# Kernel tuning notes

Hardware: AMD Instinct MI355X
Metric: run time of the kernel (lower is better)

Reference implementation:

```python
import jax, jax.numpy as jnp
import numpy as np

B, S, E, H = 2, 2048, 1024, 16
D = E // H  # head size

def setup_inputs() -> dict:
    key = jax.random.key(0)
    ks = jax.random.split(key, 11)
    s = 0.02
    return {
        "q": jax.random.normal(ks[0], (B, S, E), jnp.float32),
        "k": jax.random.normal(ks[1], (B, S, E), jnp.float32),
        "v": jax.random.normal(ks[2], (B, S, E), jnp.float32),
        "Wq": jax.random.normal(ks[3], (E, E), jnp.float32) * s,
        "bq": jax.random.normal(ks[4], (E,), jnp.float32) * s,
        "Wk": jax.random.normal(ks[5], (E, E), jnp.float32) * s,
        "bk": jax.random.normal(ks[6], (E,), jnp.float32) * s,
        "Wv": jax.random.normal(ks[7], (E, E), jnp.float32) * s,
        "bv": jax.random.normal(ks[8], (E,), jnp.float32) * s,
        "Wo": jax.random.normal(ks[9], (E, E), jnp.float32) * s,
        "bo": jax.random.normal(ks[10], (E,), jnp.float32) * s,
    }

def reference(q, k, v, Wq, bq, Wk, bk, Wv, bv, Wo, bo):
    b, sq, _ = q.shape
    sk = k.shape[1]
    # linear projections, split into heads: [B,S,H,D]
    qh = (q @ Wq.T + bq).reshape(b, sq, H, D)
    kh = (k @ Wk.T + bk).reshape(b, sk, H, D)
    vh = (v @ Wv.T + bv).reshape(b, sk, H, D)
    # NOTE: original module does NOT scale by 1/sqrt(D)
    scores = jnp.einsum('bqhe,bkhe->bhqk', qh, kh)
    probs = jax.nn.softmax(scores, axis=-1)  # dropout = identity (eval)
    attn = jnp.einsum('bhqk,bkhe->bqhe', probs, vh).reshape(b, sq, E)
    return attn @ Wo.T + bo
```

## Files before the change

### kernel.cpp

```cpp
#include <hip/hip_runtime.h>
#include <stdint.h>

#define BH 2
#define SEQ 2048
#define EMB 1024
#define NH 16
#define HD 64
#define MROWS (BH * SEQ)
#define BHN (BH * NH)
#define LOG2E 1.44269504f

typedef __attribute__((ext_vector_type(8))) short bf16x8;
typedef __attribute__((ext_vector_type(4))) float f32x4;
typedef __attribute__((ext_vector_type(16))) float f32x16;

static __device__ __forceinline__ unsigned short f2bf(float x) {
  union { float f; unsigned int u; } a; a.f = x;
  unsigned int r = a.u + 0x7fffu + ((a.u >> 16) & 1u);
  return (unsigned short)(r >> 16);
}

static __device__ __forceinline__ unsigned int cvtpk(float lo, float hi) {
  unsigned int r;
  asm("v_cvt_pk_bf16_f32 %0, %1, %2" : "=v"(r) : "v"(lo), "v"(hi));
  return r;
}

static __device__ __forceinline__ float vexp2(float x) {
  float r;
  asm("v_exp_f32 %0, %1" : "=v"(r) : "v"(x));
  return r;
}

static __device__ __forceinline__ void plswap(unsigned int& a, unsigned int& b) {
  asm volatile("v_permlane32_swap_b32 %0, %1" : "+v"(a), "+v"(b));
}

struct Conv7 { const float* s[7]; unsigned short* d[7]; };

__global__ __launch_bounds__(256) void conv_all(Conv7 a) {
  const int b = blockIdx.x;
  int r, off;
  if (b < 12288) { r = b >> 12; off = b & 4095; }
  else { int t = b - 12288; r = 3 + (t >> 10); off = t & 1023; }
  const int i = (off * 256 + threadIdx.x) * 4;
  float4 v = *(const float4*)(a.s[r] + i);
  ushort4 o;
  o.x = f2bf(v.x); o.y = f2bf(v.y); o.z = f2bf(v.z); o.w = f2bf(v.w);
  *(ushort4*)(a.d[r] + i) = o;
}

struct B3 { const float* p[3]; };
struct Out3 { void* p[3]; };

template <int MODE>
__global__ __launch_bounds__(256) void gemm128(const unsigned short* __restrict__ Abase,
                                               const unsigned short* __restrict__ Bbase,
                                               B3 biases, Out3 outs) {
  __shared__ unsigned short lsm[128 * 128];
  unsigned short* lA = lsm;
  unsigned short* lB = lsm + 128 * 64;
  const int z = blockIdx.z;
  const unsigned short* A  = Abase + (size_t)z * MROWS * EMB;
  const unsigned short* Bt = Bbase + (size_t)z * EMB * EMB;
  const float* bias = biases.p[z];
  const int tid = threadIdx.x;
  const int lane = tid & 63;
  const int w = tid >> 6;
  const int row0 = blockIdx.x * 128;
  const int col0 = blockIdx.y * 128;
  const int wr = (w >> 1) * 64;
  const int wc = (w & 1) * 64;
  const int r16 = lane & 15;
  const int g = lane >> 4;

  const int s_rowoff = (lane >> 3);
  const int s_col = ((lane & 7) ^ s_rowoff) * 8;

  f32x4 acc[4][4] = {};

  for (int kt = 0; kt < EMB / 64; ++kt) {
    const int k0 = kt * 64;
    __syncthreads();
#pragma unroll
    for (int j = 0; j < 4; ++j) {
      const int chunk = w * 4 + j;
      const int row = chunk * 8 + s_rowoff;
      __builtin_amdgcn_global_load_lds(
          (const __attribute__((address_space(1))) void*)(A + (size_t)(row0 + row) * EMB + k0 + s_col),
          (__attribute__((address_space(3))) void*)(lA + chunk * 512), 16, 0, 0);
      __builtin_amdgcn_global_load_lds(
          (const __attribute__((address_space(1))) void*)(Bt + (size_t)(col0 + row) * EMB + k0 + s_col),
          (__attribute__((address_space(3))) void*)(lB + chunk * 512), 16, 0, 0);
    }
    __syncthreads();
#pragma unroll
    for (int kk = 0; kk < 2; ++kk) {
      bf16x8 a[4], b[4];
#pragma unroll
      for (int m = 0; m < 4; ++m) {
        const int row = wr + m * 16 + r16;
        a[m] = *(const bf16x8*)(lA + row * 64 + (((kk << 2) + g) ^ (r16 & 7)) * 8);
      }
#pragma unroll
      for (int n = 0; n < 4; ++n) {
        const int row = wc + n * 16 + r16;
        b[n] = *(const bf16x8*)(lB + row * 64 + (((kk << 2) + g) ^ (r16 & 7)) * 8);
      }
#pragma unroll
      for (int m = 0; m < 4; ++m)
#pragma unroll
        for (int n = 0; n < 4; ++n)
          acc[m][n] = __builtin_amdgcn_mfma_f32_16x16x32_bf16(a[m], b[n], acc[m][n], 0, 0, 0);
    }
  }

  if (MODE == 1) {
#pragma unroll
    for (int m = 0; m < 4; ++m)
#pragma unroll
      for (int n = 0; n < 4; ++n) {
        const int colg = col0 + wc + n * 16 + r16;
        const float bv = bias[colg];
#pragma unroll
        for (int j = 0; j < 4; ++j) {
          const int rowg = row0 + wr + m * 16 + g * 4 + j;
          ((float*)outs.p[0])[(size_t)rowg * EMB + colg] = acc[m][n][j] + bv;
        }
      }
  } else {
    const int b_ = row0 >> 11;
    const int s0 = row0 & 2047;
    const int h0 = col0 >> 6;
    const float scl = (z == 0) ? LOG2E : 1.0f;
    if (z != 2) {
#pragma unroll
      for (int half = 0; half < 2; ++half) {
        __syncthreads();
        if ((w >> 1) == half) {
#pragma unroll
          for (int m = 0; m < 4; ++m)
#pragma unroll
            for (int n = 0; n < 4; ++n) {
              const int cl = wc + n * 16 + r16;
              const float bv = bias[col0 + cl];
#pragma unroll
              for (int j = 0; j < 4; ++j)
                lsm[(m * 16 + g * 4 + j) * 136 + cl] = f2bf((acc[m][n][j] + bv) * scl);
            }
        }
        __syncthreads();
        const int rr_ = tid >> 2, q4 = tid & 3;
        const int h_ = h0 + (q4 >> 1);
        unsigned short* dst = (unsigned short*)outs.p[z] +
            ((size_t)(b_ * NH + h_) * SEQ + s0 + half * 64 + rr_) * 64 + (q4 & 1) * 32;
        uint4 x0 = *(uint4*)&lsm[rr_ * 136 + q4 * 32];
        uint4 x1 = *(uint4*)&lsm[rr_ * 136 + q4 * 32 + 8];
        uint4 x2 = *(uint4*)&lsm[rr_ * 136 + q4 * 32 + 16];
        uint4 x3 = *(uint4*)&lsm[rr_ * 136 + q4 * 32 + 24];
        *(uint4*)dst = x0;
        *(uint4*)(dst + 8) = x1;
        *(uint4*)(dst + 16) = x2;
        *(uint4*)(dst + 24) = x3;
      }
    } else {
#pragma unroll
      for (int half = 0; half < 2; ++half) {
        __syncthreads();
        if ((w >> 1) == half) {
#pragma unroll
          for (int m = 0; m < 4; ++m)
#pragma unroll
            for (int n = 0; n < 4; ++n) {
              const int cl = wc + n * 16 + r16;
              const float bv = bias[col0 + cl];
#pragma unroll
              for (int j = 0; j < 4; ++j)
                lsm[cl * 72 + m * 16 + g * 4 + j] = f2bf(acc[m][n][j] + bv);
            }
        }
        __syncthreads();
        const int c_ = tid >> 1, sh = tid & 1;
        const int h_ = h0 + (c_ >> 6);
        const int d_ = c_ & 63;
        unsigned short* dst = (unsigned short*)outs.p[2] +
            ((size_t)(b_ * NH + h_) * HD + d_) * SEQ + s0 + half * 64 + sh * 32;
        uint4 y0 = *(uint4*)&lsm[c_ * 72 + sh * 32];
        uint4 y1 = *(uint4*)&lsm[c_ * 72 + sh * 32 + 8];
        uint4 y2 = *(uint4*)&lsm[c_ * 72 + sh * 32 + 16];
        uint4 y3 = *(uint4*)&lsm[c_ * 72 + sh * 32 + 24];
        *(uint4*)dst = y0;
        *(uint4*)(dst + 8) = y1;
        *(uint4*)(dst + 16) = y2;
        *(uint4*)(dst + 24) = y3;
      }
    }
  }
}

__global__ __launch_bounds__(256) void attn_fwd(const unsigned short* __restrict__ Qh,
                                                const unsigned short* __restrict__ Kh,
                                                const unsigned short* __restrict__ Vt,
                                                unsigned short* __restrict__ ctx) {
  __shared__ unsigned short kbuf[2][64 * 64];
  __shared__ unsigned short vbuf[2][64 * 64];
  const int tid = threadIdx.x;
  const int lane = tid & 63;
  const int w = tid >> 6;
  const int l31 = lane & 31;
  const int hi = lane >> 5;
  const int wg = blockIdx.x;
  const int xcd = wg & 7;
  const int slot = wg >> 3;
  const int bh = xcd + 8 * (slot >> 4);
  const int qb = slot & 15;
  const size_t base = (size_t)bh * SEQ * HD;
  const unsigned short* Q = Qh + base;
  const unsigned short* K = Kh + base;
  const unsigned short* V = Vt + base;
  const int q0 = qb * 128 + w * 32;

  bf16x8 bq[4];
#pragma unroll
  for (int ks = 0; ks < 4; ++ks)
    bq[ks] = *(const bf16x8*)(Q + (size_t)(q0 + l31) * HD + ks * 16 + hi * 8);

  f32x16 oacc0 = {};
  f32x16 oacc1 = {};
  float lsum = 0.f;

  const int sr = tid >> 2;
  const int sx = (tid & 3) * 2;
  const int sd0 = ((sx) ^ (sr & 7)) * 8;
  const int sd1 = ((sx + 1) ^ (sr & 7)) * 8;

  const int NT = SEQ / 64;
  uint4 kr0, kr1, vr0, vr1;
  kr0 = *(const uint4*)(K + (size_t)sr * HD + sx * 8);
  kr1 = *(const uint4*)(K + (size_t)sr * HD + sx * 8 + 8);
  vr0 = *(const uint4*)(V + (size_t)sr * SEQ + sx * 8);
  vr1 = *(const uint4*)(V + (size_t)sr * SEQ + sx * 8 + 8);
  *(uint4*)(kbuf[0] + sr * 64 + sd0) = kr0;
  *(uint4*)(kbuf[0] + sr * 64 + sd1) = kr1;
  *(uint4*)(vbuf[0] + sr * 64 + sd0) = vr0;
  *(uint4*)(vbuf[0] + sr * 64 + sd1) = vr1;
  kr0 = *(const uint4*)(K + (size_t)(64 + sr) * HD + sx * 8);
  kr1 = *(const uint4*)(K + (size_t)(64 + sr) * HD + sx * 8 + 8);
  vr0 = *(const uint4*)(V + (size_t)sr * SEQ + 64 + sx * 8);
  vr1 = *(const uint4*)(V + (size_t)sr * SEQ + 64 + sx * 8 + 8);
  __syncthreads();

  for (int t = 0; t < NT; ++t) {
    const unsigned short* lK = kbuf[t & 1];
    const unsigned short* lV = vbuf[t & 1];
#pragma unroll
    for (int sub = 0; sub < 2; ++sub) {
      f32x16 st = {};
      __builtin_amdgcn_s_setprio(1);
#pragma unroll
      for (int ks = 0; ks < 4; ++ks) {
        bf16x8 ak = *(const bf16x8*)(lK + (sub * 32 + l31) * 64 +
                                     (((ks << 1) + hi) ^ (l31 & 7)) * 8);
        st = __builtin_amdgcn_mfma_f32_32x32x16_bf16(ak, bq[ks], st, 0, 0, 0);
      }
      __builtin_amdgcn_s_setprio(0);
      float p[16];
#pragma unroll
      for (int r = 0; r < 16; ++r) { p[r] = vexp2(st[r]); lsum += p[r]; }
#pragma unroll
      for (int h2 = 0; h2 < 2; ++h2) {
        const int b8 = h2 * 8;
        unsigned int a0 = cvtpk(p[b8 + 0], p[b8 + 1]);
        unsigned int b0 = cvtpk(p[b8 + 4], p[b8 + 5]);
        unsigned int a1 = cvtpk(p[b8 + 2], p[b8 + 3]);
        unsigned int b1 = cvtpk(p[b8 + 6], p[b8 + 7]);
        plswap(a0, b0);
        plswap(a1, b1);
        union { unsigned int u[4]; bf16x8 v; } pa;
        pa.u[0] = a0; pa.u[1] = a1; pa.u[2] = b0; pa.u[3] = b1;
        const int kst = sub * 2 + h2;
        const int vsl = (((kst << 1) + hi) ^ (l31 & 7)) * 8;
        bf16x8 v0 = *(const bf16x8*)(lV + l31 * 64 + vsl);
        bf16x8 v1 = *(const bf16x8*)(lV + (32 + l31) * 64 + vsl);
        __builtin_amdgcn_s_setprio(1);
        oacc0 = __builtin_amdgcn_mfma_f32_32x32x16_bf16(pa.v, v0, oacc0, 0, 0, 0);
        oacc1 = __builtin_amdgcn_mfma_f32_32x32x16_bf16(pa.v, v1, oacc1, 0, 0, 0);
        __builtin_amdgcn_s_setprio(0);
      }
    }
    if (t + 1 < NT) {
      unsigned short* nK = kbuf[(t + 1) & 1];
      unsigned short* nV = vbuf[(t + 1) & 1];
      *(uint4*)(nK + sr * 64 + sd0) = kr0;
      *(uint4*)(nK + sr * 64 + sd1) = kr1;
      *(uint4*)(nV + sr * 64 + sd0) = vr0;
      *(uint4*)(nV + sr * 64 + sd1) = vr1;
      if (t + 2 < NT) {
        const int kv2 = (t + 2) * 64;
        kr0 = *(const uint4*)(K + (size_t)(kv2 + sr) * HD + sx * 8);
        kr1 = *(const uint4*)(K + (size_t)(kv2 + sr) * HD + sx * 8 + 8);
        vr0 = *(const uint4*)(V + (size_t)sr * SEQ + kv2 + sx * 8);
        vr1 = *(const uint4*)(V + (size_t)sr * SEQ + kv2 + sx * 8 + 8);
      }
    }
    __syncthreads();
  }

  lsum += __shfl_xor(lsum, 32, 64);
  const float linv = 1.0f / lsum;
  const int b_ = bh >> 4, h_ = bh & 15;
#pragma unroll
  for (int reg = 0; reg < 16; ++reg) {
    const int crow = (reg & 3) + 8 * (reg >> 2) + 4 * hi;
    const float rv = __shfl(linv, crow, 64);
    const size_t rowaddr = ((size_t)(b_ * SEQ + q0 + crow) << 10) + h_ * 64 + l31;
    ctx[rowaddr]      = f2bf(oacc0[reg] * rv);
    ctx[rowaddr + 32] = f2bf(oacc1[reg] * rv);
  }
}

extern "C" void kernel_launch(void* const* d_in, const int* in_sizes, int n_in,
                              void* d_out, int out_size, void* d_ws, size_t ws_size,
                              hipStream_t stream) {
  const float* q  = (const float*)d_in[0];
  const float* k  = (const float*)d_in[1];
  const float* v  = (const float*)d_in[2];
  const float* Wq = (const float*)d_in[3];
  const float* bq = (const float*)d_in[4];
  const float* Wk = (const float*)d_in[5];
  const float* bk = (const float*)d_in[6];
  const float* Wv = (const float*)d_in[7];
  const float* bv = (const float*)d_in[8];
  const float* Wo = (const float*)d_in[9];
  const float* bo = (const float*)d_in[10];

  char* ws = (char*)d_ws;
  const size_t SZ_ACT = (size_t)MROWS * EMB * 2;
  const size_t SZ_W   = (size_t)EMB * EMB * 2;
  unsigned short* qb  = (unsigned short*)(ws);
  unsigned short* kb  = (unsigned short*)(ws + SZ_ACT);
  unsigned short* vb  = (unsigned short*)(ws + 2 * SZ_ACT);
  unsigned short* Wqb = (unsigned short*)(ws + 3 * SZ_ACT);
  unsigned short* Wob = (unsigned short*)(ws + 3 * SZ_ACT + 3 * SZ_W);
  unsigned short* Qh  = (unsigned short*)(ws + 3 * SZ_ACT + 4 * SZ_W);
  unsigned short* Kh  = (unsigned short*)(ws + 4 * SZ_ACT + 4 * SZ_W);
  unsigned short* Vt  = (unsigned short*)(ws + 5 * SZ_ACT + 4 * SZ_W);
  unsigned short* ctx = (unsigned short*)(ws + 6 * SZ_ACT + 4 * SZ_W);

  Conv7 ca;
  ca.s[0] = q;  ca.s[1] = k;  ca.s[2] = v;
  ca.s[3] = Wq; ca.s[4] = Wk; ca.s[5] = Wv; ca.s[6] = Wo;
  ca.d[0] = qb; ca.d[1] = kb; ca.d[2] = vb;
  ca.d[3] = Wqb; ca.d[4] = Wqb + EMB * EMB; ca.d[5] = Wqb + 2 * EMB * EMB; ca.d[6] = Wob;
  conv_all<<<16384, 256, 0, stream>>>(ca);

  B3 bqkv; bqkv.p[0] = bq; bqkv.p[1] = bk; bqkv.p[2] = bv;
  Out3 oqkv; oqkv.p[0] = (void*)Qh; oqkv.p[1] = (void*)Kh; oqkv.p[2] = (void*)Vt;
  gemm128<0><<<dim3(MROWS / 128, EMB / 128, 3), 256, 0, stream>>>(qb, Wqb, bqkv, oqkv);

  attn_fwd<<<512, 256, 0, stream>>>(Qh, Kh, Vt, ctx);

  B3 bout; bout.p[0] = bo; bout.p[1] = bo; bout.p[2] = bo;
  Out3 oout; oout.p[0] = d_out; oout.p[1] = d_out; oout.p[2] = d_out;
  gemm128<1><<<dim3(MROWS / 128, EMB / 128, 1), 256, 0, stream>>>(ctx, Wob, bout, oout);
}
```

Before: 231.0 us.

## Use 128x64 GEMM tiles and 128-key attention tiles with paired score MFMAs

The projection GEMMs now use a 128x64 output tile instead of 128x128, doubling the grid size for better CU occupancy and simplifying the head-scatter epilogue to a single LDS pass. The attention kernel stages 128 keys per double-buffered tile instead of 64, halving the number of barriers and issuing two independent score MFMA chains per step for more ILP. Row sums are accumulated with a tree reduction. The cost is more LDS in attention and lower A-reuse per GEMM tile.

```diff
diff --git a/kernel.cpp b/kernel.cpp
--- a/kernel.cpp
+++ b/kernel.cpp
@@ -57,7 +57,7 @@
 __global__ __launch_bounds__(256) void gemm128(const unsigned short* __restrict__ Abase,
                                                const unsigned short* __restrict__ Bbase,
                                                B3 biases, Out3 outs) {
-  __shared__ unsigned short lsm[128 * 128];
+  __shared__ unsigned short lsm[128 * 64 + 64 * 64];
   unsigned short* lA = lsm;
   unsigned short* lB = lsm + 128 * 64;
   const int z = blockIdx.z;
@@ -68,16 +68,16 @@
   const int lane = tid & 63;
   const int w = tid >> 6;
   const int row0 = blockIdx.x * 128;
-  const int col0 = blockIdx.y * 128;
+  const int col0 = blockIdx.y * 64;
   const int wr = (w >> 1) * 64;
-  const int wc = (w & 1) * 64;
+  const int wc = (w & 1) * 32;
   const int r16 = lane & 15;
   const int g = lane >> 4;
 
   const int s_rowoff = (lane >> 3);
   const int s_col = ((lane & 7) ^ s_rowoff) * 8;
 
-  f32x4 acc[4][4] = {};
+  f32x4 acc[4][2] = {};
 
   for (int kt = 0; kt < EMB / 64; ++kt) {
     const int k0 = kt * 64;
@@ -89,6 +89,11 @@
       __builtin_amdgcn_global_load_lds(
           (const __attribute__((address_space(1))) void*)(A + (size_t)(row0 + row) * EMB + k0 + s_col),
           (__attribute__((address_space(3))) void*)(lA + chunk * 512), 16, 0, 0);
+    }
+#pragma unroll
+    for (int j = 0; j < 2; ++j) {
+      const int chunk = w * 2 + j;
+      const int row = chunk * 8 + s_rowoff;
       __builtin_amdgcn_global_load_lds(
           (const __attribute__((address_space(1))) void*)(Bt + (size_t)(col0 + row) * EMB + k0 + s_col),
           (__attribute__((address_space(3))) void*)(lB + chunk * 512), 16, 0, 0);
@@ -96,21 +101,21 @@
     __syncthreads();
 #pragma unroll
     for (int kk = 0; kk < 2; ++kk) {
-      bf16x8 a[4], b[4];
+      bf16x8 a[4], b[2];
 #pragma unroll
       for (int m = 0; m < 4; ++m) {
         const int row = wr + m * 16 + r16;
         a[m] = *(const bf16x8*)(lA + row * 64 + (((kk << 2) + g) ^ (r16 & 7)) * 8);
       }
 #pragma unroll
-      for (int n = 0; n < 4; ++n) {
+      for (int n = 0; n < 2; ++n) {
         const int row = wc + n * 16 + r16;
         b[n] = *(const bf16x8*)(lB + row * 64 + (((kk << 2) + g) ^ (r16 & 7)) * 8);
       }
 #pragma unroll
       for (int m = 0; m < 4; ++m)
 #pragma unroll
-        for (int n = 0; n < 4; ++n)
+        for (int n = 0; n < 2; ++n)
           acc[m][n] = __builtin_amdgcn_mfma_f32_16x16x32_bf16(a[m], b[n], acc[m][n], 0, 0, 0);
     }
   }
@@ -119,7 +124,7 @@
 #pragma unroll
     for (int m = 0; m < 4; ++m)
 #pragma unroll
-      for (int n = 0; n < 4; ++n) {
+      for (int n = 0; n < 2; ++n) {
         const int colg = col0 + wc + n * 16 + r16;
         const float bv = bias[colg];
 #pragma unroll
@@ -131,69 +136,55 @@
   } else {
     const int b_ = row0 >> 11;
     const int s0 = row0 & 2047;
-    const int h0 = col0 >> 6;
+    const int h_ = col0 >> 6;
     const float scl = (z == 0) ? LOG2E : 1.0f;
+    __syncthreads();
     if (z != 2) {
 #pragma unroll
-      for (int half = 0; half < 2; ++half) {
-        __syncthreads();
-        if ((w >> 1) == half) {
-#pragma unroll
-          for (int m = 0; m < 4; ++m)
-#pragma unroll
-            for (int n = 0; n < 4; ++n) {
-              const int cl = wc + n * 16 + r16;
-              const float bv = bias[col0 + cl];
-#pragma unroll
-              for (int j = 0; j < 4; ++j)
-                lsm[(m * 16 + g * 4 + j) * 136 + cl] = f2bf((acc[m][n][j] + bv) * scl);
-            }
-        }
-        __syncthreads();
-        const int rr_ = tid >> 2, q4 = tid & 3;
-        const int h_ = h0 + (q4 >> 1);
-        unsigned short* dst = (unsigned short*)outs.p[z] +
-            ((size_t)(b_ * NH + h_) * SEQ + s0 + half * 64 + rr_) * 64 + (q4 & 1) * 32;
-        uint4 x0 = *(uint4*)&lsm[rr_ * 136 + q4 * 32];
-        uint4 x1 = *(uint4*)&lsm[rr_ * 136 + q4 * 32 + 8];
-        uint4 x2 = *(uint4*)&lsm[rr_ * 136 + q4 * 32 + 16];
-        uint4 x3 = *(uint4*)&lsm[rr_ * 136 + q4 * 32 + 24];
-        *(uint4*)dst = x0;
-        *(uint4*)(dst + 8) = x1;
-        *(uint4*)(dst + 16) = x2;
-        *(uint4*)(dst + 24) = x3;
-      }
+      for (int m = 0; m < 4; ++m)
+#pragma unroll
+        for (int n = 0; n < 2; ++n) {
+          const int cl = wc + n * 16 + r16;
+          const float bv = bias[col0 + cl];
+#pragma unroll
+          for (int j = 0; j < 4; ++j)
+            lsm[(wr + m * 16 + g * 4 + j) * 72 + cl] = f2bf((acc[m][n][j] + bv) * scl);
+        }
+      __syncthreads();
+      const int rr_ = tid >> 1, sh = tid & 1;
+      unsigned short* dst = (unsigned short*)outs.p[z] +
+          ((size_t)(b_ * NH + h_) * SEQ + s0 + rr_) * 64 + sh * 32;
+      uint4 x0 = *(uint4*)&lsm[rr_ * 72 + sh * 32];
+      uint4 x1 = *(uint4*)&lsm[rr_ * 72 + sh * 32 + 8];
+      uint4 x2 = *(uint4*)&lsm[rr_ * 72 + sh * 32 + 16];
+      uint4 x3 = *(uint4*)&lsm[rr_ * 72 + sh * 32 + 24];
+      *(uint4*)dst = x0;
+      *(uint4*)(dst + 8) = x1;
+      *(uint4*)(dst + 16) = x2;
+      *(uint4*)(dst + 24) = x3;
     } else {
 #pragma unroll
-      for (int half = 0; half < 2; ++half) {
-        __syncthreads();
-        if ((w >> 1) == half) {
-#pragma unroll
-          for (int m = 0; m < 4; ++m)
-#pragma unroll
-            for (int n = 0; n < 4; ++n) {
-              const int cl = wc + n * 16 + r16;
-              const float bv = bias[col0 + cl];
-#pragma unroll
-              for (int j = 0; j < 4; ++j)
-                lsm[cl * 72 + m * 16 + g * 4 + j] = f2bf(acc[m][n][j] + bv);
-            }
-        }
-        __syncthreads();
-        const int c_ = tid >> 1, sh = tid & 1;
-        const int h_ = h0 + (c_ >> 6);
-        const int d_ = c_ & 63;
-        unsigned short* dst = (unsigned short*)outs.p[2] +
-            ((size_t)(b_ * NH + h_) * HD + d_) * SEQ + s0 + half * 64 + sh * 32;
-        uint4 y0 = *(uint4*)&lsm[c_ * 72 + sh * 32];
-        uint4 y1 = *(uint4*)&lsm[c_ * 72 + sh * 32 + 8];
-        uint4 y2 = *(uint4*)&lsm[c_ * 72 + sh * 32 + 16];
-        uint4 y3 = *(uint4*)&lsm[c_ * 72 + sh * 32 + 24];
-        *(uint4*)dst = y0;
-        *(uint4*)(dst + 8) = y1;
-        *(uint4*)(dst + 16) = y2;
-        *(uint4*)(dst + 24) = y3;
-      }
+      for (int m = 0; m < 4; ++m)
+#pragma unroll
+        for (int n = 0; n < 2; ++n) {
+          const int cl = wc + n * 16 + r16;
+          const float bv = bias[col0 + cl];
+#pragma unroll
+          for (int j = 0; j < 4; ++j)
+            lsm[cl * 136 + wr + m * 16 + g * 4 + j] = f2bf(acc[m][n][j] + bv);
+        }
+      __syncthreads();
+      const int d_ = tid >> 2, q4 = tid & 3;
+      unsigned short* dst = (unsigned short*)outs.p[2] +
+          ((size_t)(b_ * NH + h_) * HD + d_) * SEQ + s0 + q4 * 32;
+      uint4 y0 = *(uint4*)&lsm[d_ * 136 + q4 * 32];
+      uint4 y1 = *(uint4*)&lsm[d_ * 136 + q4 * 32 + 8];
+      uint4 y2 = *(uint4*)&lsm[d_ * 136 + q4 * 32 + 16];
+      uint4 y3 = *(uint4*)&lsm[d_ * 136 + q4 * 32 + 24];
+      *(uint4*)dst = y0;
+      *(uint4*)(dst + 8) = y1;
+      *(uint4*)(dst + 16) = y2;
+      *(uint4*)(dst + 24) = y3;
     }
   }
 }
@@ -202,8 +193,8 @@
                                                 const unsigned short* __restrict__ Kh,
                                                 const unsigned short* __restrict__ Vt,
                                                 unsigned short* __restrict__ ctx) {
-  __shared__ unsigned short kbuf[2][64 * 64];
-  __shared__ unsigned short vbuf[2][64 * 64];
+  __shared__ unsigned short kbuf[2][128 * 64];
+  __shared__ unsigned short vbuf[2][64 * 128];
   const int tid = threadIdx.x;
   const int lane = tid & 63;
   const int w = tid >> 6;
@@ -229,78 +220,88 @@
   f32x16 oacc1 = {};
   float lsum = 0.f;
 
-  const int sr = tid >> 2;
-  const int sx = (tid & 3) * 2;
-  const int sd0 = ((sx) ^ (sr & 7)) * 8;
-  const int sd1 = ((sx + 1) ^ (sr & 7)) * 8;
-
-  const int NT = SEQ / 64;
-  uint4 kr0, kr1, vr0, vr1;
-  kr0 = *(const uint4*)(K + (size_t)sr * HD + sx * 8);
-  kr1 = *(const uint4*)(K + (size_t)sr * HD + sx * 8 + 8);
-  vr0 = *(const uint4*)(V + (size_t)sr * SEQ + sx * 8);
-  vr1 = *(const uint4*)(V + (size_t)sr * SEQ + sx * 8 + 8);
-  *(uint4*)(kbuf[0] + sr * 64 + sd0) = kr0;
-  *(uint4*)(kbuf[0] + sr * 64 + sd1) = kr1;
-  *(uint4*)(vbuf[0] + sr * 64 + sd0) = vr0;
-  *(uint4*)(vbuf[0] + sr * 64 + sd1) = vr1;
-  kr0 = *(const uint4*)(K + (size_t)(64 + sr) * HD + sx * 8);
-  kr1 = *(const uint4*)(K + (size_t)(64 + sr) * HD + sx * 8 + 8);
-  vr0 = *(const uint4*)(V + (size_t)sr * SEQ + 64 + sx * 8);
-  vr1 = *(const uint4*)(V + (size_t)sr * SEQ + 64 + sx * 8 + 8);
+  const int krow = tid >> 1, khalf = tid & 1;
+  const int vrow = tid >> 2, vq = tid & 3;
+
+  const int NT2 = SEQ / 128;
+  uint4 kr[4], vr[4];
+#pragma unroll
+  for (int i = 0; i < 4; ++i) {
+    uint4 kx = *(const uint4*)(K + (size_t)krow * HD + khalf * 32 + i * 8);
+    *(uint4*)(kbuf[0] + krow * 64 + ((khalf * 4 + i) ^ (krow & 7)) * 8) = kx;
+    uint4 vx = *(const uint4*)(V + (size_t)vrow * SEQ + vq * 32 + i * 8);
+    *(uint4*)(vbuf[0] + vrow * 128 + ((vq * 4 + i) ^ (vrow & 7)) * 8) = vx;
+  }
+#pragma unroll
+  for (int i = 0; i < 4; ++i) {
+    kr[i] = *(const uint4*)(K + (size_t)(128 + krow) * HD + khalf * 32 + i * 8);
+    vr[i] = *(const uint4*)(V + (size_t)vrow * SEQ + 128 + vq * 32 + i * 8);
+  }
   __syncthreads();
 
-  for (int t = 0; t < NT; ++t) {
+  for (int t = 0; t < NT2; ++t) {
     const unsigned short* lK = kbuf[t & 1];
     const unsigned short* lV = vbuf[t & 1];
 #pragma unroll
-    for (int sub = 0; sub < 2; ++sub) {
-      f32x16 st = {};
+    for (int pr = 0; pr < 2; ++pr) {
+      f32x16 st0 = {}, st1 = {};
       __builtin_amdgcn_s_setprio(1);
 #pragma unroll
       for (int ks = 0; ks < 4; ++ks) {
-        bf16x8 ak = *(const bf16x8*)(lK + (sub * 32 + l31) * 64 +
-                                     (((ks << 1) + hi) ^ (l31 & 7)) * 8);
-        st = __builtin_amdgcn_mfma_f32_32x32x16_bf16(ak, bq[ks], st, 0, 0, 0);
+        const int sl = ((ks << 1) + hi) ^ (l31 & 7);
+        bf16x8 ak0 = *(const bf16x8*)(lK + ((pr * 2) * 32 + l31) * 64 + sl * 8);
+        bf16x8 ak1 = *(const bf16x8*)(lK + ((pr * 2 + 1) * 32 + l31) * 64 + sl * 8);
+        st0 = __builtin_amdgcn_mfma_f32_32x32x16_bf16(ak0, bq[ks], st0, 0, 0, 0);
+        st1 = __builtin_amdgcn_mfma_f32_32x32x16_bf16(ak1, bq[ks], st1, 0, 0, 0);
       }
       __builtin_amdgcn_s_setprio(0);
-      float p[16];
-#pragma unroll
-      for (int r = 0; r < 16; ++r) { p[r] = vexp2(st[r]); lsum += p[r]; }
-#pragma unroll
-      for (int h2 = 0; h2 < 2; ++h2) {
-        const int b8 = h2 * 8;
-        unsigned int a0 = cvtpk(p[b8 + 0], p[b8 + 1]);
-        unsigned int b0 = cvtpk(p[b8 + 4], p[b8 + 5]);
-        unsigned int a1 = cvtpk(p[b8 + 2], p[b8 + 3]);
-        unsigned int b1 = cvtpk(p[b8 + 6], p[b8 + 7]);
-        plswap(a0, b0);
-        plswap(a1, b1);
-        union { unsigned int u[4]; bf16x8 v; } pa;
-        pa.u[0] = a0; pa.u[1] = a1; pa.u[2] = b0; pa.u[3] = b1;
-        const int kst = sub * 2 + h2;
-        const int vsl = (((kst << 1) + hi) ^ (l31 & 7)) * 8;
-        bf16x8 v0 = *(const bf16x8*)(lV + l31 * 64 + vsl);
-        bf16x8 v1 = *(const bf16x8*)(lV + (32 + l31) * 64 + vsl);
-        __builtin_amdgcn_s_setprio(1);
-        oacc0 = __builtin_amdgcn_mfma_f32_32x32x16_bf16(pa.v, v0, oacc0, 0, 0, 0);
-        oacc1 = __builtin_amdgcn_mfma_f32_32x32x16_bf16(pa.v, v1, oacc1, 0, 0, 0);
-        __builtin_amdgcn_s_setprio(0);
-      }
-    }
-    if (t + 1 < NT) {
+#pragma unroll
+      for (int half = 0; half < 2; ++half) {
+        const int sub = pr * 2 + half;
+        const f32x16& st = half ? st1 : st0;
+        float p[16];
+#pragma unroll
+        for (int r = 0; r < 16; ++r) p[r] = vexp2(st[r]);
+        float q01 = p[0] + p[1], q23 = p[2] + p[3], q45 = p[4] + p[5], q67 = p[6] + p[7];
+        float q89 = p[8] + p[9], qab = p[10] + p[11], qcd = p[12] + p[13], qef = p[14] + p[15];
+        lsum += ((q01 + q23) + (q45 + q67)) + ((q89 + qab) + (qcd + qef));
+#pragma unroll
+        for (int h2 = 0; h2 < 2; ++h2) {
+          const int b8 = h2 * 8;
+          unsigned int a0 = cvtpk(p[b8 + 0], p[b8 + 1]);
+          unsigned int b0 = cvtpk(p[b8 + 4], p[b8 + 5]);
+          unsigned int a1 = cvtpk(p[b8 + 2], p[b8 + 3]);
+          unsigned int b1 = cvtpk(p[b8 + 6], p[b8 + 7]);
+          plswap(a0, b0);
+          plswap(a1, b1);
+          union { unsigned int u[4]; bf16x8 v; } pa;
+          pa.u[0] = a0; pa.u[1] = a1; pa.u[2] = b0; pa.u[3] = b1;
+          const int kst = sub * 2 + h2;
+          const int s0_ = ((kst << 1) + hi);
+          bf16x8 v0 = *(const bf16x8*)(lV + l31 * 128 + (s0_ ^ (l31 & 7)) * 8);
+          bf16x8 v1 = *(const bf16x8*)(lV + (32 + l31) * 128 + (s0_ ^ (l31 & 7)) * 8);
+          __builtin_amdgcn_s_setprio(1);
+          oacc0 = __builtin_amdgcn_mfma_f32_32x32x16_bf16(pa.v, v0, oacc0, 0, 0, 0);
+          oacc1 = __builtin_amdgcn_mfma_f32_32x32x16_bf16(pa.v, v1, oacc1, 0, 0, 0);
+          __builtin_amdgcn_s_setprio(0);
+        }
+      }
+    }
+    if (t + 1 < NT2) {
       unsigned short* nK = kbuf[(t + 1) & 1];
       unsigned short* nV = vbuf[(t + 1) & 1];
-      *(uint4*)(nK + sr * 64 + sd0) = kr0;
-      *(uint4*)(nK + sr * 64 + sd1) = kr1;
-      *(uint4*)(nV + sr * 64 + sd0) = vr0;
-      *(uint4*)(nV + sr * 64 + sd1) = vr1;
-      if (t + 2 < NT) {
-        const int kv2 = (t + 2) * 64;
-        kr0 = *(const uint4*)(K + (size_t)(kv2 + sr) * HD + sx * 8);
-        kr1 = *(const uint4*)(K + (size_t)(kv2 + sr) * HD + sx * 8 + 8);
-        vr0 = *(const uint4*)(V + (size_t)sr * SEQ + kv2 + sx * 8);
-        vr1 = *(const uint4*)(V + (size_t)sr * SEQ + kv2 + sx * 8 + 8);
+#pragma unroll
+      for (int i = 0; i < 4; ++i) {
+        *(uint4*)(nK + krow * 64 + ((khalf * 4 + i) ^ (krow & 7)) * 8) = kr[i];
+        *(uint4*)(nV + vrow * 128 + ((vq * 4 + i) ^ (vrow & 7)) * 8) = vr[i];
+      }
+      if (t + 2 < NT2) {
+        const int kv2 = (t + 2) * 128;
+#pragma unroll
+        for (int i = 0; i < 4; ++i) {
+          kr[i] = *(const uint4*)(K + (size_t)(kv2 + krow) * HD + khalf * 32 + i * 8);
+          vr[i] = *(const uint4*)(V + (size_t)vrow * SEQ + kv2 + vq * 32 + i * 8);
+        }
       }
     }
     __syncthreads();
@@ -356,11 +357,11 @@
 
   B3 bqkv; bqkv.p[0] = bq; bqkv.p[1] = bk; bqkv.p[2] = bv;
   Out3 oqkv; oqkv.p[0] = (void*)Qh; oqkv.p[1] = (void*)Kh; oqkv.p[2] = (void*)Vt;
-  gemm128<0><<<dim3(MROWS / 128, EMB / 128, 3), 256, 0, stream>>>(qb, Wqb, bqkv, oqkv);
+  gemm128<0><<<dim3(MROWS / 128, EMB / 64, 3), 256, 0, stream>>>(qb, Wqb, bqkv, oqkv);
 
   attn_fwd<<<512, 256, 0, stream>>>(Qh, Kh, Vt, ctx);
 
   B3 bout; bout.p[0] = bo; bout.p[1] = bo; bout.p[2] = bo;
   Out3 oout; oout.p[0] = d_out; oout.p[1] = d_out; oout.p[2] = d_out;
-  gemm128<1><<<dim3(MROWS / 128, EMB / 128, 1), 256, 0, stream>>>(ctx, Wob, bout, oout);
-}
+  gemm128<1><<<dim3(MROWS / 128, EMB / 64, 1), 256, 0, stream>>>(ctx, Wob, bout, oout);
+}
```

Measured after the change: 241.1 us. 1.04x slower.
